# Kernel optimization log

Measured on AMD Instinct MI355X. Metric: run time of the kernel, lower is better.

## Reference

```python
import jax, jax.numpy as jnp
import numpy as np

C, H, N, B, L = 1, 512, 64, 16, 2048  # n_channels, n_heads, d_kernel, batch, seq_len


def setup_inputs() -> dict:
    key = jax.random.key(0)
    k1, k2 = jax.random.split(key)
    u = jax.random.normal(k1, (B, C * H, L), dtype=jnp.float32)
    k = jax.random.normal(k2, (C, H, N), dtype=jnp.float32)
    return {"u": u, "k": k}


def _l1_normalize(x, axis):
    # torch.linalg.norm(x, ord=1, dim=axis, keepdim=True): vector 1-norm along `axis`
    return x / jnp.sum(jnp.abs(x), axis=axis, keepdims=True)


def _forward(u, k):
    c, h, n = k.shape
    bsz, d, l = u.shape  # d == c*h
    dt = u.dtype
    # Shift matrix A: A[:, :, 1:, :-1] = I  (companion-style shift)
    A = jnp.zeros((c, h, n, n), dtype=dt).at[:, :, 1:, :-1].set(jnp.eye(n - 1, dtype=dt))
    # b = e1 broadcast to (c, h, n)
    b_vec = jnp.zeros((c, h, n), dtype=dt).at[:, :, 0].set(1.0)
    # closed-loop: k_norm = L1-normalize(clamp(k, 1/16, 1)); A_cl = L1-normalize(A + b k^T)
    k_norm = _l1_normalize(jnp.clip(k, 1.0 / 16.0, 1.0), axis=2)
    BK = jnp.einsum('chi,chj->chij', b_vec, k_norm)
    M = _l1_normalize(A + BK, axis=2)

    # Krylov recurrence: f[i] = k . (M^i b), i = 0..l-1
    def step(x, _):
        f_i = jnp.einsum('chn,chn->ch', k, x)
        x_next = jnp.einsum('chij,chj->chi', M, x)
        return x_next, f_i

    _, f = jax.lax.scan(step, b_vec, None, length=l)  # f: (l, c, h)
    f = jnp.moveaxis(f, 0, -1)  # (c, h, l)

    # Causal FFT convolution of u (b, c, h, l) with filter f (c, h, l)
    n_fft = 2 * l
    uf = jnp.fft.rfft(u.reshape(bsz, c, h, l), n=n_fft)
    ff = jnp.fft.rfft(f, n=n_fft)
    y = jnp.fft.irfft(uf * ff[None], n=n_fft)[..., :l]
    return y.reshape(bsz, c * h, l)


def reference(u, k):
    return _forward(u, k)
```

## Files before the change

### kernel.cpp

```cpp
#include <hip/hip_runtime.h>


namespace {

constexpr int kH = 512;
constexpr int kL = 2048;
constexpr int kChunks = 32;
constexpr int kStride = 68;

typedef __attribute__((ext_vector_type(8))) short bf16x8;
typedef __attribute__((ext_vector_type(4))) float f32x4;

__device__ inline unsigned short f32_to_bf16_rne(float x) {
  unsigned int u = __float_as_uint(x);
  unsigned int r = u + 0x7FFFu + ((u >> 16) & 1u);
  return (unsigned short)(r >> 16);
}
__device__ inline float bf16_as_f32(unsigned short h) {
  return __uint_as_float(((unsigned int)h) << 16);
}
__device__ inline void cvt_split8(const f32x4 a, const f32x4 b, bf16x8& fh, bf16x8& fl) {
  #pragma unroll
  for (int j = 0; j < 4; ++j) {
    unsigned short hi = f32_to_bf16_rne(a[j]);
    fh[j] = (short)hi;
    fl[j] = (short)f32_to_bf16_rne(a[j] - bf16_as_f32(hi));
  }
  #pragma unroll
  for (int j = 0; j < 4; ++j) {
    unsigned short hi = f32_to_bf16_rne(b[j]);
    fh[4 + j] = (short)hi;
    fl[4 + j] = (short)f32_to_bf16_rne(b[j] - bf16_as_f32(hi));
  }
}

#define MFMA(A, B, C) __builtin_amdgcn_mfma_f32_16x16x32_bf16((A), (B), (C), 0, 0, 0)

__global__ __launch_bounds__(256, 2)
void ssm_mfma_kernel(const float* __restrict__ u,
                     const float* __restrict__ kin,
                     float* __restrict__ y) {
  const int h    = blockIdx.x;
  const int tid  = threadIdx.x;
  const int wq   = tid >> 6;
  const int lane = tid & 63;
  const int ln16 = lane & 15;
  const int quad = lane >> 4;

  __shared__ float taps[4][128];
  __shared__ float Ebuf[16][kStride];
  __shared__ float Rbuf[16][kStride];
  __shared__ float tmpA[64], cArr[64], wArr[64], gArr[64], sArr[64];

  float kv = 0.f, kc = 0.f, kn = 0.f, cc = 0.f;
  if (tid < 64) {
    kv = kin[h * 64 + tid];
    kc = fminf(fmaxf(kv, 0.0625f), 1.0f);
    tmpA[tid] = kc;
  }
  __syncthreads();
  if (tid < 64) {
    float ks = 0.f;
    for (int j = 0; j < 64; ++j) ks += tmpA[j];
    kn = kc / ks;
    cc = 1.0f / (1.0f + kn);
    cArr[tid] = cc;
  }
  __syncthreads();
  if (tid < 64) {
    float P = 1.0f;
    for (int j = 0; j < tid; ++j) P *= cArr[j];
    wArr[tid] = (tid < 63) ? (kn * cc * P) : P;
    gArr[tid] = kv * P;
    if (tid == 0) sArr[0] = 1.0f;
  }
  __syncthreads();
  float acc_s = (tid == 0) ? 1.0f : 0.0f;
  for (int rr = 0; rr < 63; ++rr) {
    if (tid < 64) {
      const float sval = sArr[rr];
      const float coef = (tid > rr) ? wArr[tid - 1 - rr] : 0.0f;
      acc_s = fmaf(coef, sval, acc_s);
      if (tid == rr + 1) sArr[tid] = acc_s;
    }
    __syncthreads();
  }
  if (tid < 128) {
    const int n = tid;
    taps[0][n] = (n < 64) ? wArr[n] : 0.0f;
    taps[1][n] = (n >= 63) ? sArr[n - 63] : 0.0f;
    taps[2][n] = (n >= 63) ? gArr[n - 63] : 0.0f;
    taps[3][n] = (n < 63) ? gArr[n + 1] : 0.0f;
  }
  __syncthreads();

  bf16x8 fragH[4][2], fragL[4][2];
  #pragma unroll
  for (int mi = 0; mi < 4; ++mi) {
    #pragma unroll
    for (int tk = 0; tk < 2; ++tk) {
      const int n0 = 16 * wq + ln16 - (32 * tk + 8 * quad) + 63;
      bf16x8 fh, fl;
      #pragma unroll
      for (int j = 0; j < 8; ++j) {
        const int n = n0 - j;
        const float v = (n >= 0 && n < 127) ? taps[mi][n] : 0.0f;
        const unsigned short hi = f32_to_bf16_rne(v);
        fh[j] = (short)hi;
        fl[j] = (short)f32_to_bf16_rne(v - bf16_as_f32(hi));
      }
      fragH[mi][tk] = fh;
      fragL[mi][tk] = fl;
    }
  }

  bf16x8 pH[2], pL[2];
  {
    bf16x8 z;
    #pragma unroll
    for (int j = 0; j < 8; ++j) z[j] = 0;
    pH[0] = z; pH[1] = z; pL[0] = z; pL[1] = z;
  }

  const size_t gbase = ((size_t)ln16 * kH + h) * kL + 16 * wq + 4 * quad;
  const float* uptr = u + gbase;
  float* yptr = y + gbase;
  const int ewrow = 16 * wq + 4 * quad;

  f32x4 unext = *(const f32x4*)(uptr);

  for (int m = 0; m < kChunks; ++m) {
    const int t0 = m * 64;
    const f32x4 ucur = unext;
    if (m + 1 < kChunks) unext = *(const f32x4*)(uptr + (m + 1) * 64);

    f32x4 accY = {};
    #pragma unroll
    for (int tk = 0; tk < 2; ++tk) {
      accY = MFMA(fragH[3][tk], pH[tk], accY);
      accY = MFMA(fragH[3][tk], pL[tk], accY);
      accY = MFMA(fragL[3][tk], pH[tk], accY);
    }
    f32x4 accE = ucur;
    #pragma unroll
    for (int tk = 0; tk < 2; ++tk) {
      accE = MFMA(fragH[0][tk], pH[tk], accE);
      accE = MFMA(fragH[0][tk], pL[tk], accE);
      accE = MFMA(fragL[0][tk], pH[tk], accE);
    }
    *(f32x4*)&Ebuf[ln16][ewrow] = accE;
    __syncthreads();

    bf16x8 eH[2], eL[2];
    #pragma unroll
    for (int tk = 0; tk < 2; ++tk) {
      const int k0 = 8 * quad + 32 * tk;
      const f32x4 a = *(const f32x4*)&Ebuf[ln16][k0];
      const f32x4 b = *(const f32x4*)&Ebuf[ln16][k0 + 4];
      cvt_split8(a, b, eH[tk], eL[tk]);
    }
    f32x4 accR = {};
    #pragma unroll
    for (int tk = 0; tk < 2; ++tk) {
      accR = MFMA(fragH[1][tk], eH[tk], accR);
      accR = MFMA(fragH[1][tk], eL[tk], accR);
      accR = MFMA(fragL[1][tk], eH[tk], accR);
    }
    *(f32x4*)&Rbuf[ln16][ewrow] = accR;
    __syncthreads();

    #pragma unroll
    for (int tk = 0; tk < 2; ++tk) {
      const int k0 = 8 * quad + 32 * tk;
      const f32x4 a = *(const f32x4*)&Rbuf[ln16][k0];
      const f32x4 b = *(const f32x4*)&Rbuf[ln16][k0 + 4];
      cvt_split8(a, b, pH[tk], pL[tk]);
    }
    #pragma unroll
    for (int tk = 0; tk < 2; ++tk) {
      accY = MFMA(fragH[2][tk], pH[tk], accY);
      accY = MFMA(fragH[2][tk], pL[tk], accY);
      accY = MFMA(fragL[2][tk], pH[tk], accY);
    }
    *(f32x4*)(yptr + t0) = accY;
  }
}

}

extern "C" void kernel_launch(void* const* d_in, const int* in_sizes, int n_in,
                              void* d_out, int out_size, void* d_ws, size_t ws_size,
                              hipStream_t stream) {
  const float* u  = (const float*)d_in[0];
  const float* kk = (const float*)d_in[1];
  if (n_in >= 2 && in_sizes[0] < in_sizes[1]) {
    const float* t = u; u = kk; kk = t;
  }
  float* y = (float*)d_out;
  hipLaunchKernelGGL(ssm_mfma_kernel, dim3(kH), dim3(256), 0, stream, u, kk, y);
}
```

Baseline: 147.0 us.

## Precompute S*W product matrix to cut per-chunk recurrence to one barrier

Precomputes the product of the S and W Toeplitz operators once per block as a dense 64x64 matrix A. Each chunk then updates the state as R = A*p + S*u, replacing the two dependent MFMA stages and the two barriers of the old loop with one independent pair and a single barrier. A double-buffered Rbuf lets the next chunk's write proceed without a second sync. It also replaces the scalar bf16 split with packed v_cvt_pk_bf16 conversions and moves the setup prefix computations to wave shuffles. The cost is extra one-time setup MFMAs, different rounding from the precomputed A, and more registers for the u fragments.

Result: slower. 154.7 us (+5.2%).

```diff
diff --git a/kernel.cpp b/kernel.cpp
--- a/kernel.cpp
+++ b/kernel.cpp
@@ -11,30 +11,44 @@
 typedef __attribute__((ext_vector_type(8))) short bf16x8;
 typedef __attribute__((ext_vector_type(4))) float f32x4;
 
-__device__ inline unsigned short f32_to_bf16_rne(float x) {
-  unsigned int u = __float_as_uint(x);
-  unsigned int r = u + 0x7FFFu + ((u >> 16) & 1u);
-  return (unsigned short)(r >> 16);
-}
-__device__ inline float bf16_as_f32(unsigned short h) {
-  return __uint_as_float(((unsigned int)h) << 16);
-}
+#define MFMA(A, B, C) __builtin_amdgcn_mfma_f32_16x16x32_bf16((A), (B), (C), 0, 0, 0)
+
+__device__ inline unsigned int cvt_pk_bf16(float lo, float hi) {
+  unsigned int r;
+  asm("v_cvt_pk_bf16_f32 %0, %1, %2" : "=v"(r) : "v"(lo), "v"(hi));
+  return r;
+}
+
+union B8U4 { bf16x8 v; unsigned int u[4]; };
+
 __device__ inline void cvt_split8(const f32x4 a, const f32x4 b, bf16x8& fh, bf16x8& fl) {
-  #pragma unroll
-  for (int j = 0; j < 4; ++j) {
-    unsigned short hi = f32_to_bf16_rne(a[j]);
-    fh[j] = (short)hi;
-    fl[j] = (short)f32_to_bf16_rne(a[j] - bf16_as_f32(hi));
-  }
-  #pragma unroll
-  for (int j = 0; j < 4; ++j) {
-    unsigned short hi = f32_to_bf16_rne(b[j]);
-    fh[4 + j] = (short)hi;
-    fl[4 + j] = (short)f32_to_bf16_rne(b[j] - bf16_as_f32(hi));
-  }
-}
-
-#define MFMA(A, B, C) __builtin_amdgcn_mfma_f32_16x16x32_bf16((A), (B), (C), 0, 0, 0)
+  B8U4 H, L;
+  float x[8];
+  #pragma unroll
+  for (int j = 0; j < 4; ++j) { x[j] = a[j]; x[4 + j] = b[j]; }
+  #pragma unroll
+  for (int d = 0; d < 4; ++d) {
+    const float x0 = x[2 * d], x1 = x[2 * d + 1];
+    const unsigned int hp = cvt_pk_bf16(x0, x1);
+    const float h0 = __uint_as_float(hp << 16);
+    const float h1 = __uint_as_float(hp & 0xFFFF0000u);
+    H.u[d] = hp;
+    L.u[d] = cvt_pk_bf16(x0 - h0, x1 - h1);
+  }
+  fh = H.v; fl = L.v;
+}
+
+__device__ inline void gen_frag(const float* tp, int n0, bf16x8& fh, bf16x8& fl) {
+  float t[8];
+  #pragma unroll
+  for (int j = 0; j < 8; ++j) {
+    const int n = n0 - j;
+    t[j] = (n >= 0 && n < 127) ? tp[n] : 0.0f;
+  }
+  const f32x4 a = {t[0], t[1], t[2], t[3]};
+  const f32x4 b = {t[4], t[5], t[6], t[7]};
+  cvt_split8(a, b, fh, fl);
+}
 
 __global__ __launch_bounds__(256, 2)
 void ssm_mfma_kernel(const float* __restrict__ u,
@@ -47,71 +61,98 @@
   const int ln16 = lane & 15;
   const int quad = lane >> 4;
 
-  __shared__ float taps[4][128];
-  __shared__ float Ebuf[16][kStride];
-  __shared__ float Rbuf[16][kStride];
-  __shared__ float tmpA[64], cArr[64], wArr[64], gArr[64], sArr[64];
-
-  float kv = 0.f, kc = 0.f, kn = 0.f, cc = 0.f;
-  if (tid < 64) {
-    kv = kin[h * 64 + tid];
-    kc = fminf(fmaxf(kv, 0.0625f), 1.0f);
-    tmpA[tid] = kc;
+  __shared__ float sArr[64], gArr[64], wPad[128];
+  __shared__ float taps[3][128];
+  __shared__ float Abuf[64][kStride];
+  __shared__ float Rbuf[2][16][kStride];
+
+  if (wq == 0) {
+    const float kv = kin[h * 64 + lane];
+    const float kc = fminf(fmaxf(kv, 0.0625f), 1.0f);
+    float ks = kc;
+    #pragma unroll
+    for (int off = 32; off >= 1; off >>= 1) ks += __shfl_xor(ks, off);
+    const float kn = kc / ks;
+    const float cc = 1.0f / (1.0f + kn);
+    float pp = cc;
+    #pragma unroll
+    for (int off = 1; off < 64; off <<= 1) {
+      const float t = __shfl_up(pp, off);
+      if (lane >= off) pp *= t;
+    }
+    float Pe = __shfl_up(pp, 1);
+    if (lane == 0) Pe = 1.0f;
+    const float w = (lane < 63) ? (kn * cc * Pe) : Pe;
+    const float g = kv * Pe;
+    float s = (lane == 0) ? 1.0f : 0.0f;
+    for (int rr = 0; rr < 63; ++rr) {
+      const float sv = __shfl(s, rr);
+      const float cf = __shfl(w, lane - 1 - rr);
+      if (lane > rr) s = fmaf(cf, sv, s);
+    }
+    sArr[lane] = s;
+    gArr[lane] = g;
+    wPad[lane] = w;
+    wPad[lane + 64] = 0.0f;
   }
   __syncthreads();
-  if (tid < 64) {
-    float ks = 0.f;
-    for (int j = 0; j < 64; ++j) ks += tmpA[j];
-    kn = kc / ks;
-    cc = 1.0f / (1.0f + kn);
-    cArr[tid] = cc;
+
+  for (int idx = tid; idx < 384; idx += 256) {
+    const int c = idx >> 7, n = idx & 127;
+    float v;
+    if (c == 0)      v = (n >= 63 && n < 127) ? sArr[n - 63] : 0.0f;
+    else if (c == 1) v = (n >= 63 && n < 127) ? gArr[n - 63] : 0.0f;
+    else             v = (n < 63) ? gArr[n + 1] : 0.0f;
+    taps[c][n] = v;
   }
   __syncthreads();
-  if (tid < 64) {
-    float P = 1.0f;
-    for (int j = 0; j < tid; ++j) P *= cArr[j];
-    wArr[tid] = (tid < 63) ? (kn * cc * P) : P;
-    gArr[tid] = kv * P;
-    if (tid == 0) sArr[0] = 1.0f;
+
+  bf16x8 sH[2], sL[2], g2H[2], g2L[2], g1H[2], g1L[2], aH[2], aL[2];
+  #pragma unroll
+  for (int tk = 0; tk < 2; ++tk) {
+    const int n0 = 16 * wq + ln16 - (32 * tk + 8 * quad) + 63;
+    gen_frag(taps[0], n0, sH[tk], sL[tk]);
+    gen_frag(taps[1], n0, g2H[tk], g2L[tk]);
+    gen_frag(taps[2], n0, g1H[tk], g1L[tk]);
+  }
+
+  {
+    f32x4 accA[4];
+    #pragma unroll
+    for (int nt = 0; nt < 4; ++nt) accA[nt] = (f32x4){0.f, 0.f, 0.f, 0.f};
+    #pragma unroll
+    for (int nt = 0; nt < 4; ++nt) {
+      #pragma unroll
+      for (int tk = 0; tk < 2; ++tk) {
+        float t[8];
+        #pragma unroll
+        for (int j = 0; j < 8; ++j)
+          t[j] = wPad[(8 * quad + 32 * tk + j) - (16 * nt + ln16) + 63];
+        const f32x4 a = {t[0], t[1], t[2], t[3]};
+        const f32x4 b = {t[4], t[5], t[6], t[7]};
+        bf16x8 wh, wl;
+        cvt_split8(a, b, wh, wl);
+        accA[nt] = MFMA(sH[tk], wh, accA[nt]);
+        accA[nt] = MFMA(sH[tk], wl, accA[nt]);
+        accA[nt] = MFMA(sL[tk], wh, accA[nt]);
+        accA[nt] = MFMA(sL[tk], wl, accA[nt]);
+      }
+    }
+    #pragma unroll
+    for (int nt = 0; nt < 4; ++nt) {
+      #pragma unroll
+      for (int r = 0; r < 4; ++r)
+        Abuf[16 * wq + 4 * quad + r][16 * nt + ln16] = accA[nt][r];
+    }
   }
   __syncthreads();
-  float acc_s = (tid == 0) ? 1.0f : 0.0f;
-  for (int rr = 0; rr < 63; ++rr) {
-    if (tid < 64) {
-      const float sval = sArr[rr];
-      const float coef = (tid > rr) ? wArr[tid - 1 - rr] : 0.0f;
-      acc_s = fmaf(coef, sval, acc_s);
-      if (tid == rr + 1) sArr[tid] = acc_s;
-    }
-    __syncthreads();
-  }
-  if (tid < 128) {
-    const int n = tid;
-    taps[0][n] = (n < 64) ? wArr[n] : 0.0f;
-    taps[1][n] = (n >= 63) ? sArr[n - 63] : 0.0f;
-    taps[2][n] = (n >= 63) ? gArr[n - 63] : 0.0f;
-    taps[3][n] = (n < 63) ? gArr[n + 1] : 0.0f;
-  }
-  __syncthreads();
-
-  bf16x8 fragH[4][2], fragL[4][2];
-  #pragma unroll
-  for (int mi = 0; mi < 4; ++mi) {
-    #pragma unroll
-    for (int tk = 0; tk < 2; ++tk) {
-      const int n0 = 16 * wq + ln16 - (32 * tk + 8 * quad) + 63;
-      bf16x8 fh, fl;
-      #pragma unroll
-      for (int j = 0; j < 8; ++j) {
-        const int n = n0 - j;
-        const float v = (n >= 0 && n < 127) ? taps[mi][n] : 0.0f;
-        const unsigned short hi = f32_to_bf16_rne(v);
-        fh[j] = (short)hi;
-        fl[j] = (short)f32_to_bf16_rne(v - bf16_as_f32(hi));
-      }
-      fragH[mi][tk] = fh;
-      fragL[mi][tk] = fl;
-    }
+  #pragma unroll
+  for (int tk = 0; tk < 2; ++tk) {
+    const int row = 16 * wq + ln16;
+    const int k0 = 32 * tk + 8 * quad;
+    const f32x4 a = *(const f32x4*)&Abuf[row][k0];
+    const f32x4 b = *(const f32x4*)&Abuf[row][k0 + 4];
+    cvt_split8(a, b, aH[tk], aL[tk]);
   }
 
   bf16x8 pH[2], pL[2];
@@ -122,67 +163,69 @@
     pH[0] = z; pH[1] = z; pL[0] = z; pL[1] = z;
   }
 
-  const size_t gbase = ((size_t)ln16 * kH + h) * kL + 16 * wq + 4 * quad;
-  const float* uptr = u + gbase;
-  float* yptr = y + gbase;
+  const float* ub = u + ((size_t)ln16 * kH + h) * kL + 8 * quad;
+  float* yp = y + ((size_t)ln16 * kH + h) * kL + 16 * wq + 4 * quad;
   const int ewrow = 16 * wq + 4 * quad;
 
-  f32x4 unext = *(const f32x4*)(uptr);
-
+  f32x4 uv[4];
+  #pragma unroll
+  for (int i = 0; i < 4; ++i)
+    uv[i] = *(const f32x4*)(ub + 32 * (i >> 1) + 4 * (i & 1));
+
+  int buf = 0;
   for (int m = 0; m < kChunks; ++m) {
     const int t0 = m * 64;
-    const f32x4 ucur = unext;
-    if (m + 1 < kChunks) unext = *(const f32x4*)(uptr + (m + 1) * 64);
-
+    bf16x8 uH[2], uL[2];
+    cvt_split8(uv[0], uv[1], uH[0], uL[0]);
+    cvt_split8(uv[2], uv[3], uH[1], uL[1]);
+    const int tn = (m < kChunks - 1) ? t0 + 64 : t0;
+    #pragma unroll
+    for (int i = 0; i < 4; ++i)
+      uv[i] = *(const f32x4*)(ub + tn + 32 * (i >> 1) + 4 * (i & 1));
+
+    f32x4 accP = {};
+    #pragma unroll
+    for (int tk = 0; tk < 2; ++tk) {
+      accP = MFMA(aH[tk], pH[tk], accP);
+      accP = MFMA(aH[tk], pL[tk], accP);
+      accP = MFMA(aL[tk], pH[tk], accP);
+    }
+    f32x4 accU = {};
+    #pragma unroll
+    for (int tk = 0; tk < 2; ++tk) {
+      accU = MFMA(sH[tk], uH[tk], accU);
+      accU = MFMA(sH[tk], uL[tk], accU);
+      accU = MFMA(sL[tk], uH[tk], accU);
+    }
     f32x4 accY = {};
     #pragma unroll
     for (int tk = 0; tk < 2; ++tk) {
-      accY = MFMA(fragH[3][tk], pH[tk], accY);
-      accY = MFMA(fragH[3][tk], pL[tk], accY);
-      accY = MFMA(fragL[3][tk], pH[tk], accY);
-    }
-    f32x4 accE = ucur;
-    #pragma unroll
-    for (int tk = 0; tk < 2; ++tk) {
-      accE = MFMA(fragH[0][tk], pH[tk], accE);
-      accE = MFMA(fragH[0][tk], pL[tk], accE);
-      accE = MFMA(fragL[0][tk], pH[tk], accE);
-    }
-    *(f32x4*)&Ebuf[ln16][ewrow] = accE;
-    __syncthreads();
-
-    bf16x8 eH[2], eL[2];
+      accY = MFMA(g1H[tk], pH[tk], accY);
+      accY = MFMA(g1H[tk], pL[tk], accY);
+      accY = MFMA(g1L[tk], pH[tk], accY);
+    }
+    const f32x4 accR = accP + accU;
+    *(f32x4*)&Rbuf[buf][ln16][ewrow] = accR;
+    asm volatile("s_waitcnt lgkmcnt(0)" ::: "memory");
+    __builtin_amdgcn_s_barrier();
+    asm volatile("" ::: "memory");
+
     #pragma unroll
     for (int tk = 0; tk < 2; ++tk) {
       const int k0 = 8 * quad + 32 * tk;
-      const f32x4 a = *(const f32x4*)&Ebuf[ln16][k0];
-      const f32x4 b = *(const f32x4*)&Ebuf[ln16][k0 + 4];
-      cvt_split8(a, b, eH[tk], eL[tk]);
-    }
-    f32x4 accR = {};
-    #pragma unroll
-    for (int tk = 0; tk < 2; ++tk) {
-      accR = MFMA(fragH[1][tk], eH[tk], accR);
-      accR = MFMA(fragH[1][tk], eL[tk], accR);
-      accR = MFMA(fragL[1][tk], eH[tk], accR);
-    }
-    *(f32x4*)&Rbuf[ln16][ewrow] = accR;
-    __syncthreads();
-
-    #pragma unroll
-    for (int tk = 0; tk < 2; ++tk) {
-      const int k0 = 8 * quad + 32 * tk;
-      const f32x4 a = *(const f32x4*)&Rbuf[ln16][k0];
-      const f32x4 b = *(const f32x4*)&Rbuf[ln16][k0 + 4];
-      cvt_split8(a, b, pH[tk], pL[tk]);
-    }
-    #pragma unroll
-    for (int tk = 0; tk < 2; ++tk) {
-      accY = MFMA(fragH[2][tk], pH[tk], accY);
-      accY = MFMA(fragH[2][tk], pL[tk], accY);
-      accY = MFMA(fragL[2][tk], pH[tk], accY);
-    }
-    *(f32x4*)(yptr + t0) = accY;
+      const f32x4 ra = *(const f32x4*)&Rbuf[buf][ln16][k0];
+      const f32x4 rb = *(const f32x4*)&Rbuf[buf][ln16][k0 + 4];
+      cvt_split8(ra, rb, pH[tk], pL[tk]);
+    }
+    f32x4 accY2 = accY;
+    #pragma unroll
+    for (int tk = 0; tk < 2; ++tk) {
+      accY2 = MFMA(g2H[tk], pH[tk], accY2);
+      accY2 = MFMA(g2H[tk], pL[tk], accY2);
+      accY2 = MFMA(g2L[tk], pH[tk], accY2);
+    }
+    *(f32x4*)(yp + t0) = accY2;
+    buf ^= 1;
   }
 }
 
```
